# Performance work log

Hardware: AMD Instinct MI355X
Metric: run time of the kernel (lower is better)

The kernel has to match this reference:

```python
import jax, jax.numpy as jnp
import numpy as np

NUM_FIELDS = 50
CARD = 10000  # per-field cardinality; global index = x + field_offset
FACTOR_DIM = 64
ATT_SIZE = 64
BATCH = 2048


def setup_inputs() -> dict:
    key = jax.random.key(0)
    ks = jax.random.split(key, 5)
    x = jax.random.randint(ks[0], (BATCH, NUM_FIELDS), 0, CARD, dtype=jnp.int64)
    emb = jax.random.normal(ks[1], (NUM_FIELDS * CARD, FACTOR_DIM), jnp.float32) * 0.1
    W1 = jax.random.normal(ks[2], (FACTOR_DIM, ATT_SIZE), jnp.float32) * 0.1
    b1 = jnp.zeros((ATT_SIZE,), jnp.float32)
    w2 = jax.random.normal(ks[3], (ATT_SIZE, 1), jnp.float32) * 0.1
    b2 = jnp.zeros((1,), jnp.float32)
    lin_w = jax.random.normal(ks[4], (NUM_FIELDS * CARD, 1), jnp.float32) * 0.1
    lin_b = jnp.zeros((1,), jnp.float32)
    return {"x": x, "emb": emb, "W1": W1, "b1": b1, "w2": w2, "b2": b2,
            "lin_w": lin_w, "lin_b": lin_b}


def reference(x, emb, W1, b1, w2, b2, lin_w, lin_b):
    F = NUM_FIELDS
    offsets = (jnp.arange(F, dtype=x.dtype) * CARD)[None, :]  # [1, F]
    idx = x + offsets                                          # [B, F] global ids
    factors = emb[idx]                                         # [B, F, D]
    iu, ju = np.triu_indices(F, k=1)                           # P = F*(F-1)/2 pairs (i < j)
    inter = factors[:, iu, :] * factors[:, ju, :]              # [B, P, D]
    # attention MLP: Dense -> ReLU -> Dense(1) -> Softmax over pair axis
    h = jax.nn.relu(jnp.einsum('bpd,da->bpa', inter, W1) + b1)
    logits = jnp.einsum('bpa,ao->bpo', h, w2) + b2             # [B, P, 1]
    scores = jax.nn.softmax(logits, axis=1)
    inter_sum = jnp.sum(inter, axis=-1, keepdims=True)         # [B, P, 1]
    attended = jnp.sum(inter_sum * scores, axis=1)             # [B, 1]
    linear = jnp.sum(lin_w[idx], axis=1) + lin_b               # [B, 1]
    return linear + attended
```

## Files before the change

kernel.cpp:

```cpp
#include <hip/hip_runtime.h>
#include <hip/hip_bf16.h>

#define NF 50
#define NCARD 10000
#define FD 64
#define NPAIR 1225
#define NPAIR_PAD 1232
#define NTILE 77
#define FSTRIDE 68

typedef short bf16x8 __attribute__((ext_vector_type(8)));
typedef float f32x4 __attribute__((ext_vector_type(4)));

__device__ inline short f2bf(float f) {
    union { float f; unsigned u; } v; v.f = f;
    unsigned r = v.u + 0x7fffu + ((v.u >> 16) & 1u);
    return (short)(r >> 16);
}

__global__ __launch_bounds__(256) void afm_kernel(
    const int* __restrict__ x,
    const float* __restrict__ emb,
    const float* __restrict__ W1,
    const float* __restrict__ b1,
    const float* __restrict__ w2,
    const float* __restrict__ lin_w,
    const float* __restrict__ lin_b,
    float* __restrict__ out)
{
    __shared__ __align__(16) float fac[NF * FSTRIDE];
    __shared__ float plog[NPAIR_PAD];
    __shared__ float pis[NPAIR_PAD];
    __shared__ unsigned char pi8[NPAIR_PAD];
    __shared__ unsigned char pj8[NPAIR_PAD];
    __shared__ float s_red[8];
    __shared__ float s_red2[8];
    __shared__ float s_linear;

    const int b    = blockIdx.x;
    const int tid  = threadIdx.x;
    const int lane = tid & 63;
    const int wid  = tid >> 6;
    const int n16  = lane & 15;
    const int quad = lane >> 4;

    if (tid == 0) s_linear = 0.f;
    __syncthreads();

    const int* xrow = x + b * NF;
    for (int t = tid; t < NF * 16; t += 256) {
        int f = t >> 4, q = t & 15;
        int gid = xrow[f] + f * NCARD;
        const float4 v = *(const float4*)(emb + (size_t)gid * FD + (q << 2));
        *(float4*)(&fac[f * FSTRIDE + (q << 2)]) = v;
    }
    if (tid < NF) {
        int gid = xrow[tid] + tid * NCARD;
        atomicAdd(&s_linear, lin_w[gid]);
    }
    for (int p = tid; p < NPAIR_PAD; p += 256) {
        int i = 0, j = 0;
        if (p < NPAIR) {
            float disc = (float)((2 * NF - 1) * (2 * NF - 1) - 8 * p);
            i = (int)(((float)(2 * NF - 1) - sqrtf(disc)) * 0.5f);
            if (i < 0) i = 0;
            if (i > NF - 2) i = NF - 2;
            while (i + 1 <= NF - 2 && (i + 1) * (NF - 1) - ((i + 1) * i) / 2 <= p) ++i;
            while (i > 0 && i * (NF - 1) - (i * (i - 1)) / 2 > p) --i;
            j = p - (i * (NF - 1) - (i * (i - 1)) / 2) + i + 1;
        }
        pi8[p] = (unsigned char)i;
        pj8[p] = (unsigned char)j;
    }

    bf16x8 bfrag[4][2];
    float b1v[4], w2v[4];
    #pragma unroll
    for (int nt = 0; nt < 4; ++nt) {
        int a = nt * 16 + n16;
        b1v[nt] = b1[a];
        w2v[nt] = w2[a];
        #pragma unroll
        for (int ks = 0; ks < 2; ++ks) {
            bf16x8 bv;
            #pragma unroll
            for (int jj = 0; jj < 8; ++jj) {
                int k = ks * 32 + quad * 8 + jj;
                bv[jj] = f2bf(W1[k * 64 + a]);
            }
            bfrag[nt][ks] = bv;
        }
    }
    __syncthreads();

    for (int t = wid; t < NTILE; t += 4) {
        const int p0 = t * 16;
        const int p  = p0 + n16;
        const int fi = pi8[p];
        const int fj = pj8[p];
        const float* fpi = &fac[fi * FSTRIDE];
        const float* fpj = &fac[fj * FSTRIDE];

        float is = 0.f;
        bf16x8 afrag[2];
        #pragma unroll
        for (int ks = 0; ks < 2; ++ks) {
            const int k0 = ks * 32 + quad * 8;
            float4 a0 = *(const float4*)(fpi + k0);
            float4 a1 = *(const float4*)(fpi + k0 + 4);
            float4 c0 = *(const float4*)(fpj + k0);
            float4 c1 = *(const float4*)(fpj + k0 + 4);
            float v0 = a0.x * c0.x, v1 = a0.y * c0.y, v2 = a0.z * c0.z, v3 = a0.w * c0.w;
            float v4 = a1.x * c1.x, v5 = a1.y * c1.y, v6 = a1.z * c1.z, v7 = a1.w * c1.w;
            is += ((v0 + v1) + (v2 + v3)) + ((v4 + v5) + (v6 + v7));
            bf16x8 av;
            av[0] = f2bf(v0); av[1] = f2bf(v1); av[2] = f2bf(v2); av[3] = f2bf(v3);
            av[4] = f2bf(v4); av[5] = f2bf(v5); av[6] = f2bf(v6); av[7] = f2bf(v7);
            afrag[ks] = av;
        }

        float lacc[4] = {0.f, 0.f, 0.f, 0.f};
        #pragma unroll
        for (int nt = 0; nt < 4; ++nt) {
            f32x4 acc = {0.f, 0.f, 0.f, 0.f};
            acc = __builtin_amdgcn_mfma_f32_16x16x32_bf16(afrag[0], bfrag[nt][0], acc, 0, 0, 0);
            acc = __builtin_amdgcn_mfma_f32_16x16x32_bf16(afrag[1], bfrag[nt][1], acc, 0, 0, 0);
            #pragma unroll
            for (int r = 0; r < 4; ++r)
                lacc[r] += fmaxf(acc[r] + b1v[nt], 0.f) * w2v[nt];
        }
        #pragma unroll
        for (int m = 1; m <= 8; m <<= 1) {
            #pragma unroll
            for (int r = 0; r < 4; ++r) lacc[r] += __shfl_xor(lacc[r], m, 64);
        }
        if (n16 == 0) {
            int prow = p0 + (quad << 2);
            plog[prow + 0] = lacc[0];
            plog[prow + 1] = lacc[1];
            plog[prow + 2] = lacc[2];
            plog[prow + 3] = lacc[3];
        }
        is += __shfl_xor(is, 16, 64);
        is += __shfl_xor(is, 32, 64);
        if (lane < 16) pis[p] = is;
    }
    __syncthreads();

    float mx = -1e30f;
    for (int p = tid; p < NPAIR; p += 256) mx = fmaxf(mx, plog[p]);
    #pragma unroll
    for (int m = 32; m >= 1; m >>= 1) mx = fmaxf(mx, __shfl_xor(mx, m, 64));
    if (lane == 0) s_red[wid] = mx;
    __syncthreads();
    mx = fmaxf(fmaxf(s_red[0], s_red[1]), fmaxf(s_red[2], s_red[3]));
    __syncthreads();

    float se = 0.f, sei = 0.f;
    for (int p = tid; p < NPAIR; p += 256) {
        float e = __expf(plog[p] - mx);
        se  += e;
        sei += e * pis[p];
    }
    #pragma unroll
    for (int m = 32; m >= 1; m >>= 1) {
        se  += __shfl_xor(se, m, 64);
        sei += __shfl_xor(sei, m, 64);
    }
    if (lane == 0) { s_red[wid] = se; s_red2[wid] = sei; }
    __syncthreads();
    if (tid == 0) {
        float tse  = s_red[0] + s_red[1] + s_red[2] + s_red[3];
        float tsei = s_red2[0] + s_red2[1] + s_red2[2] + s_red2[3];
        out[b] = s_linear + lin_b[0] + tsei / tse;
    }
}

extern "C" void kernel_launch(void* const* d_in, const int* in_sizes, int n_in,
                              void* d_out, int out_size, void* d_ws, size_t ws_size,
                              hipStream_t stream) {
    const int*   x     = (const int*)d_in[0];
    const float* emb   = (const float*)d_in[1];
    const float* W1    = (const float*)d_in[2];
    const float* b1    = (const float*)d_in[3];
    const float* w2    = (const float*)d_in[4];
    const float* lin_w = (const float*)d_in[6];
    const float* lin_b = (const float*)d_in[7];
    float* out = (float*)d_out;
    const int batch = out_size;
    afm_kernel<<<batch, 256, 0, stream>>>(x, emb, W1, b1, w2, lin_w, lin_b, out);
}
```

Baseline: 242.9 us.

## Store factors as fp16, transpose MFMA, compute pair sums via ones-MFMA

Embeddings are converted to fp16 when staged into shared memory, and pair products are computed as packed fp16 multiplies instead of fp32 multiplies followed by manual bf16 rounding. The MFMA is transposed so W1 is the A operand, with bias folded into the accumulator init. This cuts the cross-lane reduction to two shuffles, and the per-pair factor sum comes from an extra MFMA against a ones vector. Pair indices are precomputed as packed byte offsets. The aim is fewer VALU conversions, less LDS traffic and fewer shuffles, at the cost of fp16 precision on products and sums.

```diff
diff --git a/kernel.cpp b/kernel.cpp
--- a/kernel.cpp
+++ b/kernel.cpp
@@ -7,16 +7,10 @@
 #define NPAIR 1225
 #define NPAIR_PAD 1232
 #define NTILE 77
-#define FSTRIDE 68
+#define FSH 72
 
-typedef short bf16x8 __attribute__((ext_vector_type(8)));
+typedef _Float16 h16x8 __attribute__((ext_vector_type(8)));
 typedef float f32x4 __attribute__((ext_vector_type(4)));
-
-__device__ inline short f2bf(float f) {
-    union { float f; unsigned u; } v; v.f = f;
-    unsigned r = v.u + 0x7fffu + ((v.u >> 16) & 1u);
-    return (short)(r >> 16);
-}
 
 __global__ __launch_bounds__(256) void afm_kernel(
     const int* __restrict__ x,
@@ -28,11 +22,10 @@
     const float* __restrict__ lin_b,
     float* __restrict__ out)
 {
-    __shared__ __align__(16) float fac[NF * FSTRIDE];
+    __shared__ __align__(16) _Float16 fach[NF * FSH];
     __shared__ float plog[NPAIR_PAD];
     __shared__ float pis[NPAIR_PAD];
-    __shared__ unsigned char pi8[NPAIR_PAD];
-    __shared__ unsigned char pj8[NPAIR_PAD];
+    __shared__ unsigned poff[NPAIR_PAD];
     __shared__ float s_red[8];
     __shared__ float s_red2[8];
     __shared__ float s_linear;
@@ -48,11 +41,18 @@
     __syncthreads();
 
     const int* xrow = x + b * NF;
-    for (int t = tid; t < NF * 16; t += 256) {
-        int f = t >> 4, q = t & 15;
+    for (int t = tid; t < NF * 8; t += 256) {
+        int f = t >> 3, q = t & 7;
         int gid = xrow[f] + f * NCARD;
-        const float4 v = *(const float4*)(emb + (size_t)gid * FD + (q << 2));
-        *(float4*)(&fac[f * FSTRIDE + (q << 2)]) = v;
+        const float* src = emb + (size_t)gid * FD + q * 8;
+        float4 v0 = *(const float4*)(src);
+        float4 v1 = *(const float4*)(src + 4);
+        h16x8 h;
+        h[0] = (_Float16)v0.x; h[1] = (_Float16)v0.y;
+        h[2] = (_Float16)v0.z; h[3] = (_Float16)v0.w;
+        h[4] = (_Float16)v1.x; h[5] = (_Float16)v1.y;
+        h[6] = (_Float16)v1.z; h[7] = (_Float16)v1.w;
+        *(h16x8*)(fach + f * FSH + q * 8) = h;
     }
     if (tid < NF) {
         int gid = xrow[tid] + tid * NCARD;
@@ -69,81 +69,76 @@
             while (i > 0 && i * (NF - 1) - (i * (i - 1)) / 2 > p) --i;
             j = p - (i * (NF - 1) - (i * (i - 1)) / 2) + i + 1;
         }
-        pi8[p] = (unsigned char)i;
-        pj8[p] = (unsigned char)j;
+        poff[p] = (unsigned)(i * (FSH * 2)) | ((unsigned)(j * (FSH * 2)) << 16);
     }
 
-    bf16x8 bfrag[4][2];
-    float b1v[4], w2v[4];
+    h16x8 afragW[4][2];
     #pragma unroll
-    for (int nt = 0; nt < 4; ++nt) {
-        int a = nt * 16 + n16;
-        b1v[nt] = b1[a];
-        w2v[nt] = w2[a];
+    for (int mt = 0; mt < 4; ++mt) {
+        int a = mt * 16 + n16;
         #pragma unroll
         for (int ks = 0; ks < 2; ++ks) {
-            bf16x8 bv;
+            h16x8 av;
             #pragma unroll
             for (int jj = 0; jj < 8; ++jj) {
                 int k = ks * 32 + quad * 8 + jj;
-                bv[jj] = f2bf(W1[k * 64 + a]);
+                av[jj] = (_Float16)W1[k * 64 + a];
             }
-            bfrag[nt][ks] = bv;
+            afragW[mt][ks] = av;
         }
+    }
+    h16x8 aones;
+    {
+        _Float16 o = (n16 == 0) ? (_Float16)1.0f : (_Float16)0.0f;
+        #pragma unroll
+        for (int jj = 0; jj < 8; ++jj) aones[jj] = o;
+    }
+    f32x4 b1v[4], w2v[4];
+    #pragma unroll
+    for (int mt = 0; mt < 4; ++mt) {
+        const float4 bb = *(const float4*)(b1 + mt * 16 + quad * 4);
+        const float4 ww = *(const float4*)(w2 + mt * 16 + quad * 4);
+        b1v[mt] = (f32x4){bb.x, bb.y, bb.z, bb.w};
+        w2v[mt] = (f32x4){ww.x, ww.y, ww.z, ww.w};
     }
     __syncthreads();
 
+    const char* fbase = (const char*)fach;
     for (int t = wid; t < NTILE; t += 4) {
         const int p0 = t * 16;
-        const int p  = p0 + n16;
-        const int fi = pi8[p];
-        const int fj = pj8[p];
-        const float* fpi = &fac[fi * FSTRIDE];
-        const float* fpj = &fac[fj * FSTRIDE];
+        const unsigned po = poff[p0 + n16];
+        const char* pbi = fbase + (po & 0xFFFFu) + quad * 16;
+        const char* pbj = fbase + (po >> 16) + quad * 16;
 
-        float is = 0.f;
-        bf16x8 afrag[2];
+        f32x4 acc[4];
+        #pragma unroll
+        for (int mt = 0; mt < 4; ++mt) acc[mt] = b1v[mt];
+        f32x4 accS = {0.f, 0.f, 0.f, 0.f};
+
         #pragma unroll
         for (int ks = 0; ks < 2; ++ks) {
-            const int k0 = ks * 32 + quad * 8;
-            float4 a0 = *(const float4*)(fpi + k0);
-            float4 a1 = *(const float4*)(fpi + k0 + 4);
-            float4 c0 = *(const float4*)(fpj + k0);
-            float4 c1 = *(const float4*)(fpj + k0 + 4);
-            float v0 = a0.x * c0.x, v1 = a0.y * c0.y, v2 = a0.z * c0.z, v3 = a0.w * c0.w;
-            float v4 = a1.x * c1.x, v5 = a1.y * c1.y, v6 = a1.z * c1.z, v7 = a1.w * c1.w;
-            is += ((v0 + v1) + (v2 + v3)) + ((v4 + v5) + (v6 + v7));
-            bf16x8 av;
-            av[0] = f2bf(v0); av[1] = f2bf(v1); av[2] = f2bf(v2); av[3] = f2bf(v3);
-            av[4] = f2bf(v4); av[5] = f2bf(v5); av[6] = f2bf(v6); av[7] = f2bf(v7);
-            afrag[ks] = av;
+            h16x8 fi = *(const h16x8*)(pbi + ks * 64);
+            h16x8 fj = *(const h16x8*)(pbj + ks * 64);
+            h16x8 pr = fi * fj;
+            #pragma unroll
+            for (int mt = 0; mt < 4; ++mt)
+                acc[mt] = __builtin_amdgcn_mfma_f32_16x16x32_f16(afragW[mt][ks], pr, acc[mt], 0, 0, 0);
+            accS = __builtin_amdgcn_mfma_f32_16x16x32_f16(aones, pr, accS, 0, 0, 0);
         }
 
-        float lacc[4] = {0.f, 0.f, 0.f, 0.f};
+        float lacc = 0.f;
         #pragma unroll
-        for (int nt = 0; nt < 4; ++nt) {
-            f32x4 acc = {0.f, 0.f, 0.f, 0.f};
-            acc = __builtin_amdgcn_mfma_f32_16x16x32_bf16(afrag[0], bfrag[nt][0], acc, 0, 0, 0);
-            acc = __builtin_amdgcn_mfma_f32_16x16x32_bf16(afrag[1], bfrag[nt][1], acc, 0, 0, 0);
+        for (int mt = 0; mt < 4; ++mt) {
             #pragma unroll
             for (int r = 0; r < 4; ++r)
-                lacc[r] += fmaxf(acc[r] + b1v[nt], 0.f) * w2v[nt];
+                lacc += fmaxf(acc[mt][r], 0.f) * w2v[mt][r];
         }
-        #pragma unroll
-        for (int m = 1; m <= 8; m <<= 1) {
-            #pragma unroll
-            for (int r = 0; r < 4; ++r) lacc[r] += __shfl_xor(lacc[r], m, 64);
+        lacc += __shfl_xor(lacc, 16, 64);
+        lacc += __shfl_xor(lacc, 32, 64);
+        if (lane < 16) {
+            plog[p0 + lane] = lacc;
+            pis[p0 + lane] = accS[0];
         }
-        if (n16 == 0) {
-            int prow = p0 + (quad << 2);
-            plog[prow + 0] = lacc[0];
-            plog[prow + 1] = lacc[1];
-            plog[prow + 2] = lacc[2];
-            plog[prow + 3] = lacc[3];
-        }
-        is += __shfl_xor(is, 16, 64);
-        is += __shfl_xor(is, 32, 64);
-        if (lane < 16) pis[p] = is;
     }
     __syncthreads();
 
```

After: 218.9 us. -9.9%, faster.
